# Kernel tuning notes

Hardware: AMD Instinct MI355X
Metric: run time of the kernel (lower is better)

## Reference

```python
import jax, jax.numpy as jnp
import numpy as np

D1, D2, K = 2, 4, 2   # dilation1, dilation2, kernel_size
EPS = 1e-5            # BatchNorm eps (torch default)


def _dilated_nodes(queue, dilation, new_node):
    # queue: (L, bs, C, 1); take every `dilation`-th entry, append new node,
    # lay out as (bs, C, k) then flatten to (bs, C*k) matching torch's
    # cat(..., axis=2).reshape(bs, -1).
    nodes = jnp.concatenate([queue[0::dilation], new_node[None]], axis=0)  # (k, bs, C, 1)
    bs = new_node.shape[0]
    return jnp.moveaxis(nodes[..., 0], 0, -1).reshape(bs, -1)  # (bs, C*k)


def _bn_eval(h, scale, bias, mean, var):
    return (h - mean) * (scale * jax.lax.rsqrt(var + EPS)) + bias


def setup_inputs() -> dict:
    key = jax.random.key(0)
    ks = jax.random.split(key, 17)
    bs, din, mid, out = 16384, 512, 1024, 512
    in_ch = din * K          # 1024
    return {
        "x": jax.random.normal(ks[0], (bs, din, 1), jnp.float32),
        "conv1_queue": jax.random.normal(ks[1], (D1 * (K - 1), bs, din, 1), jnp.float32),
        "conv2_queue": jax.random.normal(ks[2], (D2 * (K - 1), bs, mid, 1), jnp.float32),
        "w1": jax.random.normal(ks[3], (mid, in_ch), jnp.float32) / np.sqrt(in_ch),
        "b1": jax.random.normal(ks[4], (mid,), jnp.float32) * 0.01,
        "w2": jax.random.normal(ks[5], (out, mid * K), jnp.float32) / np.sqrt(mid * K),
        "b2": jax.random.normal(ks[6], (out,), jnp.float32) * 0.01,
        "w_skip": jax.random.normal(ks[7], (out, in_ch), jnp.float32) / np.sqrt(in_ch),
        "b_skip": jax.random.normal(ks[8], (out,), jnp.float32) * 0.01,
        "bn1_scale": jax.random.uniform(ks[9], (mid,), jnp.float32, 0.5, 1.5),
        "bn1_bias": jax.random.normal(ks[10], (mid,), jnp.float32) * 0.01,
        "bn1_mean": jax.random.normal(ks[11], (mid,), jnp.float32) * 0.1,
        "bn1_var": jax.random.uniform(ks[12], (mid,), jnp.float32, 0.5, 1.5),
        "bn2_scale": jax.random.uniform(ks[13], (out,), jnp.float32, 0.5, 1.5),
        "bn2_bias": jax.random.normal(ks[14], (out,), jnp.float32) * 0.01,
        "bn2_mean": jax.random.normal(ks[15], (out,), jnp.float32) * 0.1,
        "bn2_var": jax.random.uniform(ks[16], (out,), jnp.float32, 0.5, 1.5),
    }


def reference(x, conv1_queue, conv2_queue, w1, b1, w2, b2, w_skip, b_skip,
              bn1_scale, bn1_bias, bn1_mean, bn1_var,
              bn2_scale, bn2_bias, bn2_mean, bn2_var):
    # l1_input: (bs, in_ch) = (bs, din*K)
    l1_input = _dilated_nodes(conv1_queue, D1, x)
    conv1_out = l1_input @ w1.T + b1                       # (bs, mid)
    conv1_out = _bn_eval(jax.nn.relu(conv1_out), bn1_scale, bn1_bias, bn1_mean, bn1_var)

    # l2_input: (bs, mid*K)
    l2_input = _dilated_nodes(conv2_queue, D2, conv1_out[:, :, None])
    conv2_out = l2_input @ w2.T + b2                       # (bs, out)
    conv2_out = conv2_out + (l1_input @ w_skip.T + b_skip)  # skip (in_ch != out_ch)
    conv2_out = jax.nn.relu(conv2_out)
    conv2_out = _bn_eval(conv2_out, bn2_scale, bn2_bias, bn2_mean, bn2_var)
    return conv2_out[:, :, None]                           # (bs, out, 1)
```

## Files before the change

### kernel.cpp

```cpp
#include <hip/hip_runtime.h>
#include <hip/hip_bf16.h>


#define BS   16384
#define DIN  512
#define MID  1024
#define NOUT 512
#define KA2  3072
#define BN_EPS 1e-5f

typedef __attribute__((ext_vector_type(8))) short bf16x8;
typedef __attribute__((ext_vector_type(4))) float floatx4;

#define GLDS(g, l) __builtin_amdgcn_global_load_lds( \
    (const __attribute__((address_space(1))) void*)(g), \
    (__attribute__((address_space(3))) void*)(l), 16, 0, 0)

__device__ __forceinline__ void cvt_store8(const float* __restrict__ src,
                                           __hip_bfloat16* __restrict__ dst) {
    float4 u = *(const float4*)src;
    float4 v = *(const float4*)(src + 4);
    __hip_bfloat16 tmp[8] __attribute__((aligned(16)));
    tmp[0] = __float2bfloat16(u.x); tmp[1] = __float2bfloat16(u.y);
    tmp[2] = __float2bfloat16(u.z); tmp[3] = __float2bfloat16(u.w);
    tmp[4] = __float2bfloat16(v.x); tmp[5] = __float2bfloat16(v.y);
    tmp[6] = __float2bfloat16(v.z); tmp[7] = __float2bfloat16(v.w);
    *(float4*)dst = *(const float4*)tmp;
}

__device__ __forceinline__ void cvt_store8_s2(const float* __restrict__ src,
                                              __hip_bfloat16* __restrict__ dst) {
    __hip_bfloat16 tmp[8] __attribute__((aligned(16)));
#pragma unroll
    for (int i = 0; i < 8; ++i) tmp[i] = __float2bfloat16(src[2 * i]);
    *(float4*)dst = *(const float4*)tmp;
}

#define T_Q2  ((long)BS * 128)
#define T_Q1X ((long)BS * 64)
#define T_W1  (1024L * 1024 / 8)
#define T_W2  (512L * 3072 / 8)
#define T_ALL (T_Q2 + T_Q1X + T_W1 + T_W2)

__global__ __launch_bounds__(256) void prep_all_kernel(
    const float* __restrict__ x, const float* __restrict__ q1,
    const float* __restrict__ q2, const float* __restrict__ w1,
    const float* __restrict__ w2, const float* __restrict__ wsk,
    __hip_bfloat16* __restrict__ A2,
    __hip_bfloat16* __restrict__ w1p, __hip_bfloat16* __restrict__ w2p)
{
    long id = (long)blockIdx.x * 256 + threadIdx.x;
    if (id < T_Q2) {
        long b = id >> 7;
        int j = (int)(id & 127) << 3;
        cvt_store8(q2 + b * MID + j, A2 + b * KA2 + j);
    } else if (id < T_Q2 + T_Q1X) {
        long id2 = id - T_Q2;
        long b = id2 >> 6;
        int j = (int)(id2 & 63) << 3;
        cvt_store8(q1 + b * DIN + j, A2 + b * KA2 + 2048 + j);
        cvt_store8(x  + b * DIN + j, A2 + b * KA2 + 2560 + j);
    } else if (id < T_Q2 + T_Q1X + T_W1) {
        long t = id - (T_Q2 + T_Q1X);
        long o8 = t * 8;
        int m = (int)(o8 >> 10), k0 = (int)(o8 & 1023);
        const float* src = w1 + m * 1024 + ((k0 < 512) ? 2 * k0 : 2 * (k0 - 512) + 1);
        cvt_store8_s2(src, w1p + o8);
    } else {
        long t = id - (T_Q2 + T_Q1X + T_W1);
        long o8 = t * 8;
        int o = (int)(o8 / 3072), k0 = (int)(o8 - (long)o * 3072);
        const float* src;
        if (k0 < 1024)      src = w2 + o * 2048 + 2 * k0;
        else if (k0 < 2048) src = w2 + o * 2048 + 2 * (k0 - 1024) + 1;
        else if (k0 < 2560) src = wsk + o * 1024 + 2 * (k0 - 2048);
        else                src = wsk + o * 1024 + 2 * (k0 - 2560) + 1;
        cvt_store8_s2(src, w2p + o8);
    }
}


#define PBAR() do { __builtin_amdgcn_sched_barrier(0); \
                    __builtin_amdgcn_s_barrier(); \
                    __builtin_amdgcn_sched_barrier(0); } while (0)
#define LGKM0() asm volatile("s_waitcnt lgkmcnt(0)" ::: "memory")
#define VMW(n)  asm volatile("s_waitcnt vmcnt(" #n ")" ::: "memory")


#define STAGE_TILE(G, STRIDE, ROWBLK, K0, LBASE) do { \
    _Pragma("unroll") for (int c_ = 0; c_ < 4; ++c_) { \
        int f0_ = (c_ * 8 + wave) * 64; \
        int f_  = f0_ + lane; \
        int sr_ = f_ >> 3, cc_ = f_ & 7; \
        GLDS((G) + (size_t)((ROWBLK) + sr_) * (STRIDE) + (K0) + ((cc_ ^ (sr_ & 7)) << 3), \
             ((short*)(LBASE)) + f0_ * 8); \
    } } while (0)

#define READ_A(BUF, IH) do { \
    _Pragma("unroll") for (int i_ = 0; i_ < 4; ++i_) { \
        int r_ = wm * 128 + (IH) * 64 + i_ * 16 + (lane & 15); \
        _Pragma("unroll") for (int kk_ = 0; kk_ < 2; ++kk_) { \
            int cc_ = (kk_ * 4 + (lane >> 4)) ^ (r_ & 7); \
            a[i_][kk_] = *(const bf16x8*)&As[BUF][r_][cc_ * 8]; \
        } } } while (0)

#define READ_B(BUF, JH) do { \
    _Pragma("unroll") for (int j_ = 0; j_ < 2; ++j_) { \
        int r_ = wn * 64 + (JH) * 32 + j_ * 16 + (lane & 15); \
        _Pragma("unroll") for (int kk_ = 0; kk_ < 2; ++kk_) { \
            int cc_ = (kk_ * 4 + (lane >> 4)) ^ (r_ & 7); \
            b[(JH) * 2 + j_][kk_] = *(const bf16x8*)&Bs[BUF][r_][cc_ * 8]; \
        } } } while (0)

#define MFMA_Q(IH, JH) do { \
    __builtin_amdgcn_s_setprio(1); \
    _Pragma("unroll") for (int i_ = 0; i_ < 4; ++i_) \
    _Pragma("unroll") for (int j_ = 0; j_ < 2; ++j_) \
    _Pragma("unroll") for (int kk_ = 0; kk_ < 2; ++kk_) \
        acc[(IH) * 4 + i_][(JH) * 2 + j_] = __builtin_amdgcn_mfma_f32_16x16x32_bf16( \
            a[i_][kk_], b[(JH) * 2 + j_][kk_], acc[(IH) * 4 + i_][(JH) * 2 + j_], 0, 0, 0); \
    __builtin_amdgcn_s_setprio(0); \
} while (0)

__global__ __launch_bounds__(512, 2) void gemm1_8ph(
    const __hip_bfloat16* __restrict__ Ag,
    const __hip_bfloat16* __restrict__ Bg,
    const float* __restrict__ bias,
    const float* __restrict__ bn_s, const float* __restrict__ bn_b,
    const float* __restrict__ bn_m, const float* __restrict__ bn_v,
    __hip_bfloat16* __restrict__ hout)
{
    __shared__ __align__(16) short As[2][256][64];
    __shared__ __align__(16) short Bs[2][256][64];

    const int t = threadIdx.x;
    const int lane = t & 63;
    const int wave = t >> 6;
    const int wm = wave >> 2;
    const int wn = wave & 3;

    const int p = blockIdx.x;
    const int m0 = ((p & 7) + 8 * ((p >> 3) & 7)) * 256;
    const int n0 = (p >> 6) * 256;

    floatx4 acc[8][4];
#pragma unroll
    for (int i = 0; i < 8; ++i)
#pragma unroll
        for (int j = 0; j < 4; ++j)
            acc[i][j] = (floatx4){0.f, 0.f, 0.f, 0.f};

    bf16x8 a[4][2], b[4][2];

    STAGE_TILE(Bg, 1024, n0, 0,  Bs[0]);
    STAGE_TILE(Ag, KA2,  m0, 0,  As[0]);
    STAGE_TILE(Bg, 1024, n0, 64, Bs[1]);
    STAGE_TILE(Ag, KA2,  m0, 64, As[1]);
    VMW(0);
    __builtin_amdgcn_s_barrier();

    for (int it = 0; it < 8; ++it) {
        const bool more = (it < 7);
        const int kn = it * 128 + 128;

        READ_A(0, 0); READ_B(0, 0);
        PBAR(); LGKM0(); MFMA_Q(0, 0); PBAR();
        READ_B(0, 1);
        PBAR(); LGKM0(); MFMA_Q(0, 1); PBAR();
        READ_A(0, 1);
        if (more) STAGE_TILE(Bg, 1024, n0, kn, Bs[0]);
        PBAR(); LGKM0(); MFMA_Q(1, 1); PBAR();
        if (more) { VMW(4); } else { VMW(0); }
        if (more) STAGE_TILE(Ag, KA2, m0, kn, As[0]);
        PBAR(); MFMA_Q(1, 0); PBAR();

        READ_A(1, 0); READ_B(1, 0);
        PBAR(); LGKM0(); MFMA_Q(0, 0); PBAR();
        READ_B(1, 1);
        PBAR(); LGKM0(); MFMA_Q(0, 1); PBAR();
        READ_A(1, 1);
        if (more) STAGE_TILE(Bg, 1024, n0, kn + 64, Bs[1]);
        PBAR(); LGKM0(); MFMA_Q(1, 1); PBAR();
        VMW(4);
        if (more) STAGE_TILE(Ag, KA2, m0, kn + 64, As[1]);
        PBAR(); MFMA_Q(1, 0); PBAR();
    }

#pragma unroll
    for (int j = 0; j < 4; ++j) {
        int col = n0 + wn * 64 + j * 16 + (lane & 15);
        float bias_v = bias[col];
        float scale = bn_s[col] * rsqrtf(bn_v[col] + BN_EPS);
        float mean = bn_m[col], beta = bn_b[col];
#pragma unroll
        for (int i = 0; i < 8; ++i) {
            int rbase = m0 + wm * 128 + i * 16 + (lane >> 4) * 4;
#pragma unroll
            for (int r = 0; r < 4; ++r) {
                float v = acc[i][j][r] + bias_v;
                v = fmaxf(v, 0.f);
                v = (v - mean) * scale + beta;
                hout[(size_t)(rbase + r) * KA2 + col] = __float2bfloat16(v);
            }
        }
    }
}


#define STAGE_A2T(K0, LBASE) do { \
    _Pragma("unroll") for (int c_ = 0; c_ < 4; ++c_) { \
        int f0_ = (c_ * 8 + wave) * 64; \
        int f_  = f0_ + lane; \
        int sr_ = f_ >> 3, cc_ = f_ & 7; \
        GLDS(Ag + (size_t)(m0 + sr_) * KA2 + (K0) + ((cc_ ^ (sr_ & 7)) << 3), \
             ((short*)(LBASE)) + f0_ * 8); \
    } } while (0)

#define STAGE_B2T(K0, LBASE) do { \
    _Pragma("unroll") for (int c_ = 0; c_ < 2; ++c_) { \
        int f0_ = (c_ * 8 + wave) * 64; \
        int f_  = f0_ + lane; \
        int sr_ = f_ >> 3, cc_ = f_ & 7; \
        GLDS(Bg + (size_t)(n0 + sr_) * KA2 + (K0) + ((cc_ ^ (sr_ & 7)) << 3), \
             ((short*)(LBASE)) + f0_ * 8); \
    } } while (0)

#define READ_A2G(BUF, IH) do { \
    _Pragma("unroll") for (int i_ = 0; i_ < 4; ++i_) { \
        int r_ = wm * 128 + (IH) * 64 + i_ * 16 + (lane & 15); \
        _Pragma("unroll") for (int kk_ = 0; kk_ < 2; ++kk_) { \
            int cc_ = (kk_ * 4 + (lane >> 4)) ^ (r_ & 7); \
            a[i_][kk_] = *(const bf16x8*)&As2[BUF][r_][cc_ * 8]; \
        } } } while (0)

#define READ_B2G(BUF) do { \
    _Pragma("unroll") for (int j_ = 0; j_ < 2; ++j_) { \
        int r_ = wn * 32 + j_ * 16 + (lane & 15); \
        _Pragma("unroll") for (int kk_ = 0; kk_ < 2; ++kk_) { \
            int cc_ = (kk_ * 4 + (lane >> 4)) ^ (r_ & 7); \
            br[j_][kk_] = *(const bf16x8*)&Bs2[BUF][r_][cc_ * 8]; \
        } } } while (0)

#define MFMA_H(IH) do { \
    __builtin_amdgcn_s_setprio(1); \
    _Pragma("unroll") for (int i_ = 0; i_ < 4; ++i_) \
    _Pragma("unroll") for (int j_ = 0; j_ < 2; ++j_) \
    _Pragma("unroll") for (int kk_ = 0; kk_ < 2; ++kk_) \
        acc[(IH) * 4 + i_][j_] = __builtin_amdgcn_mfma_f32_16x16x32_bf16( \
            a[i_][kk_], br[j_][kk_], acc[(IH) * 4 + i_][j_], 0, 0, 0); \
    __builtin_amdgcn_s_setprio(0); \
} while (0)

__global__ __launch_bounds__(512, 2) void gemm2_8ph(
    const __hip_bfloat16* __restrict__ Ag,
    const __hip_bfloat16* __restrict__ Bg,
    const float* __restrict__ bias_a, const float* __restrict__ bias_b,
    const float* __restrict__ bn_s, const float* __restrict__ bn_b,
    const float* __restrict__ bn_m, const float* __restrict__ bn_v,
    float* __restrict__ fout)
{
    __shared__ __align__(16) short As2[2][256][64];
    __shared__ __align__(16) short Bs2[2][128][64];

    const int t = threadIdx.x;
    const int lane = t & 63;
    const int wave = t >> 6;
    const int wm = wave >> 2;
    const int wn = wave & 3;

    const int p = blockIdx.x;
    const int m0 = ((p & 7) + 8 * ((p >> 3) & 7)) * 256;
    const int n0 = (p >> 6) * 128;

    floatx4 acc[8][2];
#pragma unroll
    for (int i = 0; i < 8; ++i)
#pragma unroll
        for (int j = 0; j < 2; ++j)
            acc[i][j] = (floatx4){0.f, 0.f, 0.f, 0.f};

    bf16x8 a[4][2], br[2][2];

    STAGE_B2T(0,  Bs2[0]);
    STAGE_A2T(0,  As2[0]);
    STAGE_B2T(64, Bs2[1]);
    VMW(0);
    __builtin_amdgcn_s_barrier();

    for (int it = 0; it < 24; ++it) {
        const bool more = (it < 23);
        const int kn = it * 128;

        VMW(2);
        READ_A2G(0, 0); READ_B2G(0);
        STAGE_A2T(kn + 64, As2[1]);
        PBAR(); LGKM0(); MFMA_H(0); PBAR();
        READ_A2G(0, 1);
        if (more) STAGE_B2T(kn + 128, Bs2[0]);
        PBAR(); LGKM0(); MFMA_H(1); PBAR();
        if (more) { VMW(2); } else { VMW(0); }
        READ_A2G(1, 0); READ_B2G(1);
        if (more) STAGE_A2T(kn + 128, As2[0]);
        PBAR(); LGKM0(); MFMA_H(0); PBAR();
        READ_A2G(1, 1);
        if (more) STAGE_B2T(kn + 192, Bs2[1]);
        PBAR(); LGKM0(); MFMA_H(1); PBAR();
    }

#pragma unroll
    for (int j = 0; j < 2; ++j) {
        int col = n0 + wn * 32 + j * 16 + (lane & 15);
        float bias_v = bias_a[col] + bias_b[col];
        float scale = bn_s[col] * rsqrtf(bn_v[col] + BN_EPS);
        float mean = bn_m[col], beta = bn_b[col];
#pragma unroll
        for (int i = 0; i < 8; ++i) {
            int rbase = m0 + wm * 128 + i * 16 + (lane >> 4) * 4;
#pragma unroll
            for (int r = 0; r < 4; ++r) {
                float v = acc[i][j][r] + bias_v;
                v = fmaxf(v, 0.f);
                v = (v - mean) * scale + beta;
                fout[(size_t)(rbase + r) * NOUT + col] = v;
            }
        }
    }
}

extern "C" void kernel_launch(void* const* d_in, const int* in_sizes, int n_in,
                              void* d_out, int out_size, void* d_ws, size_t ws_size,
                              hipStream_t stream) {
    const float* x   = (const float*)d_in[0];
    const float* q1  = (const float*)d_in[1];
    const float* q2  = (const float*)d_in[2];
    const float* w1  = (const float*)d_in[3];
    const float* b1  = (const float*)d_in[4];
    const float* w2  = (const float*)d_in[5];
    const float* b2  = (const float*)d_in[6];
    const float* wsk = (const float*)d_in[7];
    const float* bsk = (const float*)d_in[8];
    const float* s1  = (const float*)d_in[9];
    const float* bb1 = (const float*)d_in[10];
    const float* m1  = (const float*)d_in[11];
    const float* v1  = (const float*)d_in[12];
    const float* s2  = (const float*)d_in[13];
    const float* bb2 = (const float*)d_in[14];
    const float* m2  = (const float*)d_in[15];
    const float* v2  = (const float*)d_in[16];
    float* out = (float*)d_out;

    size_t needA2 = (size_t)BS * KA2 * sizeof(__hip_bfloat16);
    size_t needW  = ((size_t)1024 * 1024 + (size_t)512 * 3072) * sizeof(__hip_bfloat16);
    char* base;
    if (ws_size >= needA2 + needW)
        base = (char*)d_ws;
    else
        base = (char*)d_in[2] + (size_t)BS * MID * sizeof(float);
    __hip_bfloat16* A2  = (__hip_bfloat16*)base;
    __hip_bfloat16* w1p = (__hip_bfloat16*)(base + needA2);
    __hip_bfloat16* w2p = w1p + 1024 * 1024;

    prep_all_kernel<<<dim3((int)(T_ALL / 256)), dim3(256), 0, stream>>>(
        x, q1, q2, w1, w2, wsk, A2, w1p, w2p);

    gemm1_8ph<<<dim3(256), dim3(512), 0, stream>>>(
        A2 + 2048, w1p, b1, s1, bb1, m1, v1, A2 + 1024);

    gemm2_8ph<<<dim3(256), dim3(512), 0, stream>>>(
        A2, w2p, b2, bsk, s2, bb2, m2, v2, out);
}
```

Baseline: 516.7 us.

## Triple-buffer A tiles in GEMM2 to deepen global-to-LDS prefetch

Adds a third LDS buffer for the A operand of the second GEMM and restructures the K loop into six-tile rotations, so A tiles are staged two iterations ahead instead of one. The wait count on outstanding vector memory loads is relaxed, letting more global-to-LDS loads stay in flight while MFMAs run. This raises LDS use per block (A grows from 64 KB to 96 KB of shorts) and may cut occupancy at the two-blocks-per-CU launch bound.

```diff
diff --git a/kernel.cpp b/kernel.cpp
--- a/kernel.cpp
+++ b/kernel.cpp
@@ -251,6 +251,17 @@
     __builtin_amdgcn_s_setprio(0); \
 } while (0)
 
+#define TILE2(T, BA, BB) do { \
+    const bool st_ = ((T) + 2 < 48); \
+    READ_A2G(BA, 0); READ_B2G(BB); \
+    if (st_) STAGE_A2T(((T) + 2) * 64, As2[((BA) + 2) % 3]); \
+    PBAR(); LGKM0(); MFMA_H(0); PBAR(); \
+    READ_A2G(BA, 1); \
+    if (st_) STAGE_B2T(((T) + 2) * 64, Bs2[BB]); \
+    if (st_) { VMW(6); } else { VMW(0); } \
+    PBAR(); LGKM0(); MFMA_H(1); PBAR(); \
+} while (0)
+
 __global__ __launch_bounds__(512, 2) void gemm2_8ph(
     const __hip_bfloat16* __restrict__ Ag,
     const __hip_bfloat16* __restrict__ Bg,
@@ -259,7 +270,7 @@
     const float* __restrict__ bn_m, const float* __restrict__ bn_v,
     float* __restrict__ fout)
 {
-    __shared__ __align__(16) short As2[2][256][64];
+    __shared__ __align__(16) short As2[3][256][64];
     __shared__ __align__(16) short Bs2[2][128][64];
 
     const int t = threadIdx.x;
@@ -284,27 +295,19 @@
     STAGE_B2T(0,  Bs2[0]);
     STAGE_A2T(0,  As2[0]);
     STAGE_B2T(64, Bs2[1]);
-    VMW(0);
+    STAGE_A2T(64, As2[1]);
+    VMW(6);
     __builtin_amdgcn_s_barrier();
 
-    for (int it = 0; it < 24; ++it) {
-        const bool more = (it < 23);
-        const int kn = it * 128;
-
-        VMW(2);
-        READ_A2G(0, 0); READ_B2G(0);
-        STAGE_A2T(kn + 64, As2[1]);
-        PBAR(); LGKM0(); MFMA_H(0); PBAR();
-        READ_A2G(0, 1);
-        if (more) STAGE_B2T(kn + 128, Bs2[0]);
-        PBAR(); LGKM0(); MFMA_H(1); PBAR();
-        if (more) { VMW(2); } else { VMW(0); }
-        READ_A2G(1, 0); READ_B2G(1);
-        if (more) STAGE_A2T(kn + 128, As2[0]);
-        PBAR(); LGKM0(); MFMA_H(0); PBAR();
-        READ_A2G(1, 1);
-        if (more) STAGE_B2T(kn + 192, Bs2[1]);
-        PBAR(); LGKM0(); MFMA_H(1); PBAR();
+#pragma unroll 1
+    for (int s = 0; s < 8; ++s) {
+        const int kt = s * 6;
+        TILE2(kt + 0, 0, 0);
+        TILE2(kt + 1, 1, 1);
+        TILE2(kt + 2, 2, 0);
+        TILE2(kt + 3, 0, 1);
+        TILE2(kt + 4, 1, 0);
+        TILE2(kt + 5, 2, 1);
     }
 
 #pragma unroll
```

Result: no change. 515.6 us (-0.2%).
